# Optimization experiments

Hardware: AMD Instinct MI355X
Metric: run time of the kernel (lower is better)

The kernel has to match this reference:

```python
import jax, jax.numpy as jnp
import numpy as np

N_SRC = 100000
N_DST = 20000
E = 640000
IN_FEATS = 256
NUM_HEADS = 4
OUT_FEATS = 32
NEG_SLOPE = 0.2


def setup_inputs() -> dict:
    key = jax.random.key(0)
    ks = jax.random.split(key, 8)
    x = jax.random.normal(ks[0], (N_SRC, IN_FEATS), dtype=jnp.float32)
    src_idx = jax.random.randint(ks[1], (E,), 0, N_SRC)
    dst_idx = jax.random.randint(ks[2], (E,), 0, N_DST)
    dst_to_src = jax.random.randint(ks[3], (N_DST,), 0, N_SRC)
    # parameters (xavier-ish scale)
    W = jax.random.normal(ks[4], (IN_FEATS, NUM_HEADS * OUT_FEATS), dtype=jnp.float32) * (1.0 / np.sqrt(IN_FEATS))
    attn_l = jax.random.normal(ks[5], (NUM_HEADS, OUT_FEATS), dtype=jnp.float32) * 0.1
    attn_r = jax.random.normal(ks[6], (NUM_HEADS, OUT_FEATS), dtype=jnp.float32) * 0.1
    return {"x": x, "W": W, "attn_l": attn_l, "attn_r": attn_r,
            "src_idx": src_idx, "dst_idx": dst_idx, "dst_to_src": dst_to_src}


def reference(x, W, attn_l, attn_r, src_idx, dst_idx, dst_to_src):
    # fc + reshape to heads: [N_src, H, D]
    h = (x @ W).reshape(N_SRC, NUM_HEADS, OUT_FEATS)
    # per-src-node left attention score: [N_src, H]
    el = jnp.einsum('nhd,hd->nh', h, attn_l)
    # self_gather: dst nodes are a subset of src nodes
    h_dst = h[dst_to_src]                       # [N_dst, H, D]
    er = jnp.einsum('nhd,hd->nh', h_dst, attn_r)  # [N_dst, H]
    # apply_edge + leaky_relu: per-edge scores [E, H]
    e = el[src_idx] + er[dst_idx]
    e = jnp.where(e >= 0, e, NEG_SLOPE * e)
    # NOTE: original code normalizes leaky_relu(e) directly (no exp)
    sum_e = jax.ops.segment_sum(e, dst_idx, num_segments=N_DST)  # [N_dst, H]
    attention = e / sum_e[dst_idx]              # [E, H]
    # attention_gather: weighted scatter-add of src features to dst
    msg = attention[:, :, None] * h[src_idx]    # [E, H, D]
    out = jax.ops.segment_sum(msg, dst_idx, num_segments=N_DST)  # [N_dst, H, D]
    return out
```

## Files before the change

### kernel.cpp

```cpp
#include <hip/hip_runtime.h>

#define N_SRC 100000
#define N_DST 20000
#define NE 640000
#define IN_F 256
#define NH 4
#define DF 32
#define NCOL 128

__global__ void k_prep(const float* __restrict__ W,
                       const float* __restrict__ attn_l,
                       const float* __restrict__ attn_r,
                       double* __restrict__ Wlr_t) {
    int k = threadIdx.x;
    for (int j = 0; j < 8; ++j) {
        const float* attn = (j < 4) ? attn_l : attn_r;
        int hh = j & 3;
        double s = 0.0;
        for (int d = 0; d < DF; ++d)
            s += (double)W[k * NCOL + hh * DF + d] * (double)attn[hh * DF + d];
        Wlr_t[(size_t)j * IN_F + k] = s;
    }
}

__global__ __launch_bounds__(512) void k_gemm(const float* __restrict__ x,
                                              const float* __restrict__ W,
                                              const double* __restrict__ Wlr_t,
                                              const int* __restrict__ dst_idx,
                                              float* __restrict__ h,
                                              double* __restrict__ el,
                                              int* __restrict__ cnt) {
    __shared__ float xs[64][68];
    __shared__ double wlds[4][66];
    const int tid = threadIdx.x;
    const int row0 = blockIdx.x * 64;
    const int lane = tid & 63;
    const int cg = __builtin_amdgcn_readfirstlane(tid >> 6);
    const int c0 = cg * 16;
    const int srow = tid >> 3;
    const int shh = tid & 3;
    const int shalf = (tid >> 2) & 1;

    float4 acc0 = make_float4(0.f, 0.f, 0.f, 0.f);
    float4 acc1 = make_float4(0.f, 0.f, 0.f, 0.f);
    float4 acc2 = make_float4(0.f, 0.f, 0.f, 0.f);
    float4 acc3 = make_float4(0.f, 0.f, 0.f, 0.f);
    double sacc = 0.0;

    for (int chunk = 0; chunk < 4; ++chunk) {
        const int kbase = chunk * 64;
        if (chunk) __syncthreads();
#pragma unroll
        for (int t = 0; t < 2; ++t) {
            int i = t * 512 + tid;
            int r = i >> 4;
            int q = i & 15;
            int row = row0 + r;
            float4 v = make_float4(0.f, 0.f, 0.f, 0.f);
            if (row < N_SRC)
                v = *((const float4*)(x + (size_t)row * IN_F + kbase + q * 4));
            *((float4*)&xs[r][q * 4]) = v;
        }
        if (tid < 256)
            wlds[tid >> 6][tid & 63] = Wlr_t[(size_t)(tid >> 6) * IN_F + kbase + (tid & 63)];
        __syncthreads();

#pragma unroll 1
        for (int kq = 0; kq < 64; kq += 4) {
            const float* wp = W + (size_t)(kbase + kq) * NCOL + c0;
            float4 r0a = *((const float4*)(wp + 0));
            float4 r0b = *((const float4*)(wp + 4));
            float4 r0c = *((const float4*)(wp + 8));
            float4 r0d = *((const float4*)(wp + 12));
            float4 r1a = *((const float4*)(wp + NCOL + 0));
            float4 r1b = *((const float4*)(wp + NCOL + 4));
            float4 r1c = *((const float4*)(wp + NCOL + 8));
            float4 r1d = *((const float4*)(wp + NCOL + 12));
            float4 r2a = *((const float4*)(wp + 2 * NCOL + 0));
            float4 r2b = *((const float4*)(wp + 2 * NCOL + 4));
            float4 r2c = *((const float4*)(wp + 2 * NCOL + 8));
            float4 r2d = *((const float4*)(wp + 2 * NCOL + 12));
            float4 r3a = *((const float4*)(wp + 3 * NCOL + 0));
            float4 r3b = *((const float4*)(wp + 3 * NCOL + 4));
            float4 r3c = *((const float4*)(wp + 3 * NCOL + 8));
            float4 r3d = *((const float4*)(wp + 3 * NCOL + 12));
            float4 xv = *((const float4*)&xs[lane][kq]);
            acc0.x += xv.x * r0a.x + xv.y * r1a.x + xv.z * r2a.x + xv.w * r3a.x;
            acc0.y += xv.x * r0a.y + xv.y * r1a.y + xv.z * r2a.y + xv.w * r3a.y;
            acc0.z += xv.x * r0a.z + xv.y * r1a.z + xv.z * r2a.z + xv.w * r3a.z;
            acc0.w += xv.x * r0a.w + xv.y * r1a.w + xv.z * r2a.w + xv.w * r3a.w;
            acc1.x += xv.x * r0b.x + xv.y * r1b.x + xv.z * r2b.x + xv.w * r3b.x;
            acc1.y += xv.x * r0b.y + xv.y * r1b.y + xv.z * r2b.y + xv.w * r3b.y;
            acc1.z += xv.x * r0b.z + xv.y * r1b.z + xv.z * r2b.z + xv.w * r3b.z;
            acc1.w += xv.x * r0b.w + xv.y * r1b.w + xv.z * r2b.w + xv.w * r3b.w;
            acc2.x += xv.x * r0c.x + xv.y * r1c.x + xv.z * r2c.x + xv.w * r3c.x;
            acc2.y += xv.x * r0c.y + xv.y * r1c.y + xv.z * r2c.y + xv.w * r3c.y;
            acc2.z += xv.x * r0c.z + xv.y * r1c.z + xv.z * r2c.z + xv.w * r3c.z;
            acc2.w += xv.x * r0c.w + xv.y * r1c.w + xv.z * r2c.w + xv.w * r3c.w;
            acc3.x += xv.x * r0d.x + xv.y * r1d.x + xv.z * r2d.x + xv.w * r3d.x;
            acc3.y += xv.x * r0d.y + xv.y * r1d.y + xv.z * r2d.y + xv.w * r3d.y;
            acc3.z += xv.x * r0d.z + xv.y * r1d.z + xv.z * r2d.z + xv.w * r3d.z;
            acc3.w += xv.x * r0d.w + xv.y * r1d.w + xv.z * r2d.w + xv.w * r3d.w;
        }

        {
            const int kb = shalf * 32;
#pragma unroll 4
            for (int k = 0; k < 32; k += 4) {
                float4 xv = *((const float4*)&xs[srow][kb + k]);
                double2 wa = *((const double2*)&wlds[shh][kb + k]);
                double2 wb = *((const double2*)&wlds[shh][kb + k + 2]);
                sacc += (double)xv.x * wa.x + (double)xv.y * wa.y
                      + (double)xv.z * wb.x + (double)xv.w * wb.y;
            }
        }
    }

    {
        int row = row0 + lane;
        if (row < N_SRC) {
            float* hp = h + (size_t)row * NCOL + c0;
            *((float4*)(hp + 0)) = acc0;
            *((float4*)(hp + 4)) = acc1;
            *((float4*)(hp + 8)) = acc2;
            *((float4*)(hp + 12)) = acc3;
        }
    }

    sacc += __shfl_xor(sacc, 4);
    {
        int row = row0 + srow;
        if (shalf == 0 && row < N_SRC)
            el[(size_t)row * NH + shh] = sacc;
    }

    for (int e = blockIdx.x * 512 + tid; e < NE; e += gridDim.x * 512)
        atomicAdd(cnt + dst_idx[e], 1);
}

__global__ __launch_bounds__(1024) void k_scan(const int* __restrict__ cnt,
                                               int* __restrict__ offsets,
                                               int* __restrict__ cursor) {
    __shared__ int wsum[16];
    __shared__ int carry;
    int tid = threadIdx.x, lane = tid & 63, w = tid >> 6;
    if (tid == 0) carry = 0;
    __syncthreads();
    for (int base = 0; base < N_DST; base += 1024) {
        int i = base + tid;
        int v = (i < N_DST) ? cnt[i] : 0;
        int s = v;
#pragma unroll
        for (int off = 1; off < 64; off <<= 1) {
            int t = __shfl_up(s, off);
            if (lane >= off) s += t;
        }
        if (lane == 63) wsum[w] = s;
        __syncthreads();
        int wprefix = 0;
        for (int k = 0; k < w; ++k) wprefix += wsum[k];
        int incl = s + wprefix + carry;
        if (i < N_DST) {
            offsets[i + 1] = incl;
            cursor[i] = 0;
        }
        __syncthreads();
        if (tid == 1023) carry = incl;
        __syncthreads();
    }
    if (tid == 0) offsets[0] = 0;
}

__global__ __launch_bounds__(256) void k_fill(const int* __restrict__ src_idx,
                                              const int* __restrict__ dst_idx,
                                              const int* __restrict__ offsets,
                                              int* __restrict__ cursor,
                                              int* __restrict__ edge_src) {
    int gid = blockIdx.x * 256 + threadIdx.x;
    if (gid >= NE) return;
    int d = dst_idx[gid];
    int pos = offsets[d] + atomicAdd(cursor + d, 1);
    edge_src[pos] = src_idx[gid];
}

__global__ __launch_bounds__(256) void k_fused(const int* __restrict__ offsets,
                                               const int* __restrict__ edge_src,
                                               const double* __restrict__ el,
                                               const float* __restrict__ x,
                                               const double* __restrict__ Wlr_t,
                                               const int* __restrict__ dst_to_src,
                                               const float* __restrict__ h,
                                               float* __restrict__ out) {
    __shared__ double att_sh[4][4][68];
    __shared__ int    s_sh[4][64];

    const int w = threadIdx.x >> 6;
    const int lane = threadIdx.x & 63;
    const int d = blockIdx.x * 4 + w;
    if (d >= N_DST) return;
    const int beg = offsets[d];
    const int deg = offsets[d + 1] - beg;

    double er4[NH];
    {
        const int srcrow = dst_to_src[d];
        float4 xv = *((const float4*)(x + (size_t)srcrow * IN_F + lane * 4));
        const double xd[4] = {(double)xv.x, (double)xv.y, (double)xv.z, (double)xv.w};
#pragma unroll
        for (int hh = 0; hh < 4; ++hh) {
            const double* wp = Wlr_t + (size_t)(4 + hh) * IN_F + lane * 4;
            er4[hh] = xd[0] * wp[0] + xd[1] * wp[1] + xd[2] * wp[2] + xd[3] * wp[3];
        }
#pragma unroll
        for (int hh = 0; hh < 4; ++hh) {
#pragma unroll
            for (int m = 32; m >= 1; m >>= 1)
                er4[hh] += __shfl_xor(er4[hh], m);
        }
    }
    const double er0 = er4[0], er1 = er4[1], er2 = er4[2], er3 = er4[3];

    double sum0 = 0.0, sum1 = 0.0, sum2 = 0.0, sum3 = 0.0;
    double e0r = 0.0, e1r = 0.0, e2r = 0.0, e3r = 0.0;
    int s_first = 0;
    for (int j = lane; j < deg; j += 64) {
        int s = edge_src[beg + j];
        double2 ela = *((const double2*)(el + (size_t)s * NH));
        double2 elb = *((const double2*)(el + (size_t)s * NH + 2));
        double e0 = ela.x + er0; e0 = (e0 >= 0.0) ? e0 : 0.2 * e0;
        double e1 = ela.y + er1; e1 = (e1 >= 0.0) ? e1 : 0.2 * e1;
        double e2 = elb.x + er2; e2 = (e2 >= 0.0) ? e2 : 0.2 * e2;
        double e3 = elb.y + er3; e3 = (e3 >= 0.0) ? e3 : 0.2 * e3;
        sum0 += e0; sum1 += e1; sum2 += e2; sum3 += e3;
        if (j == lane) { s_first = s; e0r = e0; e1r = e1; e2r = e2; e3r = e3; }
    }
#pragma unroll
    for (int m = 32; m >= 1; m >>= 1) {
        sum0 += __shfl_xor(sum0, m);
        sum1 += __shfl_xor(sum1, m);
        sum2 += __shfl_xor(sum2, m);
        sum3 += __shfl_xor(sum3, m);
    }

    if (lane < deg) {
        s_sh[w][lane] = s_first;
        att_sh[w][0][lane] = e0r / sum0;
        att_sh[w][1][lane] = e1r / sum1;
        att_sh[w][2][lane] = e2r / sum2;
        att_sh[w][3][lane] = e3r / sum3;
    }

    const int js = lane >> 5;
    const int cq = lane & 31;
    const int hd = cq >> 3;
    const double Shd = (hd == 0) ? sum0 : (hd == 1) ? sum1 : (hd == 2) ? sum2 : sum3;
    const double erhd = (hd == 0) ? er0 : (hd == 1) ? er1 : (hd == 2) ? er2 : er3;

    double acc0 = 0.0, acc1 = 0.0, acc2 = 0.0, acc3 = 0.0;
    for (int j = js; j < deg; j += 2) {
        int s; double att;
        if (j < 64) {
            s = s_sh[w][j];
            att = att_sh[w][hd][j];
        } else {
            s = edge_src[beg + j];
            double e = el[(size_t)s * NH + hd] + erhd;
            e = (e >= 0.0) ? e : 0.2 * e;
            att = e / Shd;
        }
        float4 hv = *((const float4*)(h + (size_t)s * NCOL + cq * 4));
        acc0 += att * (double)hv.x;
        acc1 += att * (double)hv.y;
        acc2 += att * (double)hv.z;
        acc3 += att * (double)hv.w;
    }
    acc0 += __shfl_xor(acc0, 32);
    acc1 += __shfl_xor(acc1, 32);
    acc2 += __shfl_xor(acc2, 32);
    acc3 += __shfl_xor(acc3, 32);

    if (lane < 32) {
        *((float4*)(out + (size_t)d * NCOL + lane * 4)) =
            make_float4((float)acc0, (float)acc1, (float)acc2, (float)acc3);
    }
}

extern "C" void kernel_launch(void* const* d_in, const int* in_sizes, int n_in,
                              void* d_out, int out_size, void* d_ws, size_t ws_size,
                              hipStream_t stream) {
    const float* x      = (const float*)d_in[0];
    const float* W      = (const float*)d_in[1];
    const float* attn_l = (const float*)d_in[2];
    const float* attn_r = (const float*)d_in[3];
    const int* src_idx  = (const int*)d_in[4];
    const int* dst_idx  = (const int*)d_in[5];
    const int* dst_to_src = (const int*)d_in[6];
    float* out = (float*)d_out;

    char* p = (char*)d_ws;
    double* Wlr_t  = (double*)p;  p += (size_t)8 * IN_F * sizeof(double);
    double* el     = (double*)p;  p += (size_t)N_SRC * NH * sizeof(double);
    float*  h      = (float*)p;   p += (size_t)N_SRC * NCOL * sizeof(float);
    int*    cnt      = (int*)p;   p += (size_t)N_DST * sizeof(int);
    int*    offsets  = (int*)p;   p += (size_t)(N_DST + 1) * sizeof(int);
    int*    cursor   = (int*)p;   p += (size_t)N_DST * sizeof(int);
    int*    edge_src = (int*)p;   p += (size_t)NE * sizeof(int);

    hipMemsetAsync(cnt, 0, (size_t)N_DST * sizeof(int), stream);

    k_prep<<<1, 256, 0, stream>>>(W, attn_l, attn_r, Wlr_t);
    k_gemm<<<(N_SRC + 63) / 64, 512, 0, stream>>>(x, W, Wlr_t, dst_idx, h, el, cnt);
    k_scan<<<1, 1024, 0, stream>>>(cnt, offsets, cursor);
    k_fill<<<(NE + 255) / 256, 256, 0, stream>>>(src_idx, dst_idx, offsets, cursor, edge_src);
    k_fused<<<N_DST / 4, 256, 0, stream>>>(offsets, edge_src, el, x, Wlr_t, dst_to_src, h, out);
}
```

Before: 263.7 us.

## Defer softmax-like normalization to end and register-prefetch GEMM x chunks

The fused aggregation kernel drops the separate pass that summed the leaky-relu scores and staged attention weights in LDS. It now accumulates the unnormalized weighted sum and the score sum together in one pass, then divides once at the end. The GEMM kernel also prefetches the next k-chunk of x and Wlr into registers while computing the current one, to overlap global loads with math. The deferred division changes rounding slightly and relies on the segment sum being nonzero. Each lane now also loads el per edge instead of reading shared memory.

```diff
diff --git a/kernel.cpp b/kernel.cpp
--- a/kernel.cpp
+++ b/kernel.cpp
@@ -41,29 +41,44 @@
     const int shh = tid & 3;
     const int shalf = (tid >> 2) & 1;
 
+    const int r_a = tid >> 4;
+    const int r_b = 32 + (tid >> 4);
+    const int q4 = (tid & 15) * 4;
+    const int wj = tid >> 6, wk = tid & 63;
+
     float4 acc0 = make_float4(0.f, 0.f, 0.f, 0.f);
     float4 acc1 = make_float4(0.f, 0.f, 0.f, 0.f);
     float4 acc2 = make_float4(0.f, 0.f, 0.f, 0.f);
     float4 acc3 = make_float4(0.f, 0.f, 0.f, 0.f);
     double sacc = 0.0;
 
+    float4 pf0 = make_float4(0.f, 0.f, 0.f, 0.f);
+    float4 pf1 = make_float4(0.f, 0.f, 0.f, 0.f);
+    double pfw = 0.0;
+    if (row0 + r_a < N_SRC)
+        pf0 = *((const float4*)(x + (size_t)(row0 + r_a) * IN_F + q4));
+    if (row0 + r_b < N_SRC)
+        pf1 = *((const float4*)(x + (size_t)(row0 + r_b) * IN_F + q4));
+    if (tid < 256)
+        pfw = Wlr_t[(size_t)wj * IN_F + wk];
+
     for (int chunk = 0; chunk < 4; ++chunk) {
         const int kbase = chunk * 64;
         if (chunk) __syncthreads();
-#pragma unroll
-        for (int t = 0; t < 2; ++t) {
-            int i = t * 512 + tid;
-            int r = i >> 4;
-            int q = i & 15;
-            int row = row0 + r;
-            float4 v = make_float4(0.f, 0.f, 0.f, 0.f);
-            if (row < N_SRC)
-                v = *((const float4*)(x + (size_t)row * IN_F + kbase + q * 4));
-            *((float4*)&xs[r][q * 4]) = v;
-        }
-        if (tid < 256)
-            wlds[tid >> 6][tid & 63] = Wlr_t[(size_t)(tid >> 6) * IN_F + kbase + (tid & 63)];
-        __syncthreads();
+        *((float4*)&xs[r_a][q4]) = pf0;
+        *((float4*)&xs[r_b][q4]) = pf1;
+        if (tid < 256) wlds[wj][wk] = pfw;
+        __syncthreads();
+
+        if (chunk < 3) {
+            const int nk = kbase + 64;
+            if (row0 + r_a < N_SRC)
+                pf0 = *((const float4*)(x + (size_t)(row0 + r_a) * IN_F + nk + q4));
+            if (row0 + r_b < N_SRC)
+                pf1 = *((const float4*)(x + (size_t)(row0 + r_b) * IN_F + nk + q4));
+            if (tid < 256)
+                pfw = Wlr_t[(size_t)wj * IN_F + nk + wk];
+        }
 
 #pragma unroll 1
         for (int kq = 0; kq < 64; kq += 4) {
@@ -191,12 +206,8 @@
                                                const int* __restrict__ dst_to_src,
                                                const float* __restrict__ h,
                                                float* __restrict__ out) {
-    __shared__ double att_sh[4][4][68];
-    __shared__ int    s_sh[4][64];
-
-    const int w = threadIdx.x >> 6;
     const int lane = threadIdx.x & 63;
-    const int d = blockIdx.x * 4 + w;
+    const int d = blockIdx.x * 4 + (threadIdx.x >> 6);
     if (d >= N_DST) return;
     const int beg = offsets[d];
     const int deg = offsets[d + 1] - beg;
@@ -218,70 +229,37 @@
                 er4[hh] += __shfl_xor(er4[hh], m);
         }
     }
-    const double er0 = er4[0], er1 = er4[1], er2 = er4[2], er3 = er4[3];
-
-    double sum0 = 0.0, sum1 = 0.0, sum2 = 0.0, sum3 = 0.0;
-    double e0r = 0.0, e1r = 0.0, e2r = 0.0, e3r = 0.0;
-    int s_first = 0;
-    for (int j = lane; j < deg; j += 64) {
-        int s = edge_src[beg + j];
-        double2 ela = *((const double2*)(el + (size_t)s * NH));
-        double2 elb = *((const double2*)(el + (size_t)s * NH + 2));
-        double e0 = ela.x + er0; e0 = (e0 >= 0.0) ? e0 : 0.2 * e0;
-        double e1 = ela.y + er1; e1 = (e1 >= 0.0) ? e1 : 0.2 * e1;
-        double e2 = elb.x + er2; e2 = (e2 >= 0.0) ? e2 : 0.2 * e2;
-        double e3 = elb.y + er3; e3 = (e3 >= 0.0) ? e3 : 0.2 * e3;
-        sum0 += e0; sum1 += e1; sum2 += e2; sum3 += e3;
-        if (j == lane) { s_first = s; e0r = e0; e1r = e1; e2r = e2; e3r = e3; }
-    }
-#pragma unroll
-    for (int m = 32; m >= 1; m >>= 1) {
-        sum0 += __shfl_xor(sum0, m);
-        sum1 += __shfl_xor(sum1, m);
-        sum2 += __shfl_xor(sum2, m);
-        sum3 += __shfl_xor(sum3, m);
-    }
-
-    if (lane < deg) {
-        s_sh[w][lane] = s_first;
-        att_sh[w][0][lane] = e0r / sum0;
-        att_sh[w][1][lane] = e1r / sum1;
-        att_sh[w][2][lane] = e2r / sum2;
-        att_sh[w][3][lane] = e3r / sum3;
-    }
 
     const int js = lane >> 5;
     const int cq = lane & 31;
     const int hd = cq >> 3;
-    const double Shd = (hd == 0) ? sum0 : (hd == 1) ? sum1 : (hd == 2) ? sum2 : sum3;
-    const double erhd = (hd == 0) ? er0 : (hd == 1) ? er1 : (hd == 2) ? er2 : er3;
-
+    const double erhd = (hd == 0) ? er4[0] : (hd == 1) ? er4[1]
+                       : (hd == 2) ? er4[2] : er4[3];
+
+    double sp = 0.0;
     double acc0 = 0.0, acc1 = 0.0, acc2 = 0.0, acc3 = 0.0;
     for (int j = js; j < deg; j += 2) {
-        int s; double att;
-        if (j < 64) {
-            s = s_sh[w][j];
-            att = att_sh[w][hd][j];
-        } else {
-            s = edge_src[beg + j];
-            double e = el[(size_t)s * NH + hd] + erhd;
-            e = (e >= 0.0) ? e : 0.2 * e;
-            att = e / Shd;
-        }
+        int s = edge_src[beg + j];
+        double e = el[(size_t)s * NH + hd] + erhd;
+        e = (e >= 0.0) ? e : 0.2 * e;
+        sp += e;
         float4 hv = *((const float4*)(h + (size_t)s * NCOL + cq * 4));
-        acc0 += att * (double)hv.x;
-        acc1 += att * (double)hv.y;
-        acc2 += att * (double)hv.z;
-        acc3 += att * (double)hv.w;
-    }
+        acc0 += e * (double)hv.x;
+        acc1 += e * (double)hv.y;
+        acc2 += e * (double)hv.z;
+        acc3 += e * (double)hv.w;
+    }
+    sp   += __shfl_xor(sp, 32);
     acc0 += __shfl_xor(acc0, 32);
     acc1 += __shfl_xor(acc1, 32);
     acc2 += __shfl_xor(acc2, 32);
     acc3 += __shfl_xor(acc3, 32);
 
+    const double inv = (deg > 0) ? 1.0 / sp : 0.0;
     if (lane < 32) {
         *((float4*)(out + (size_t)d * NCOL + lane * 4)) =
-            make_float4((float)acc0, (float)acc1, (float)acc2, (float)acc3);
+            make_float4((float)(acc0 * inv), (float)(acc1 * inv),
+                        (float)(acc2 * inv), (float)(acc3 * inv));
     }
 }
 
```

After: 261.3 us. About the same (-0.9%).
